# Performance work log

Hardware: AMD Instinct MI355X
Metric: run time of the kernel (lower is better)

## Reference

```python
import jax, jax.numpy as jnp
import numpy as np

B, S, D_MODEL, H = 2, 2048, 1024, 16
DIMS = D_MODEL // H  # 64


def setup_inputs() -> dict:
    key = jax.random.key(0)
    ks = jax.random.split(key, 7)
    scale = 1.0 / np.sqrt(D_MODEL)
    x = jax.random.normal(ks[0], (B, S, D_MODEL), dtype=jnp.float32)
    # Stacked per-head projection params: nn.Linear(d_model, dims) per head
    Wq = jax.random.uniform(ks[1], (H, DIMS, D_MODEL), minval=-scale, maxval=scale, dtype=jnp.float32)
    Wk = jax.random.uniform(ks[2], (H, DIMS, D_MODEL), minval=-scale, maxval=scale, dtype=jnp.float32)
    Wv = jax.random.uniform(ks[3], (H, DIMS, D_MODEL), minval=-scale, maxval=scale, dtype=jnp.float32)
    bq = jax.random.uniform(ks[4], (H, DIMS), minval=-scale, maxval=scale, dtype=jnp.float32)
    bk = jax.random.uniform(ks[5], (H, DIMS), minval=-scale, maxval=scale, dtype=jnp.float32)
    bv = jax.random.uniform(ks[6], (H, DIMS), minval=-scale, maxval=scale, dtype=jnp.float32)
    return {"x": x, "Wq": Wq, "Wk": Wk, "Wv": Wv, "bq": bq, "bk": bk, "bv": bv}


def reference(x, Wq, Wk, Wv, bq, bk, bv):
    # Per-head linear projections: [B,S,D] x [H,E,D] -> [B,H,S,E]
    q = jnp.einsum('bsd,hed->bhse', x, Wq) + bq[None, :, None, :]
    k = jnp.einsum('bsd,hed->bhse', x, Wk) + bk[None, :, None, :]
    v = jnp.einsum('bsd,hed->bhse', x, Wv) + bv[None, :, None, :]
    norm = DIMS ** (-0.5)
    # (q @ k^T) * norm @ v  -- NO softmax, as in the source
    scores = jnp.einsum('bhse,bhte->bhst', q, k) * norm  # [B,H,S,S]
    out = jnp.einsum('bhst,bhte->bhse', scores, v)       # [B,H,S,E]
    # concat heads along feature dim (head order matches torch.cat)
    return out.transpose(0, 2, 1, 3).reshape(B, S, H * DIMS)
```

## Files before the change

kernel.cpp:

```cpp
#include <hip/hip_runtime.h>


typedef __attribute__((ext_vector_type(8))) __bf16 bf16x8;
typedef __attribute__((ext_vector_type(8))) short short8;
typedef __attribute__((ext_vector_type(4))) float f32x4;
typedef __attribute__((ext_vector_type(4))) unsigned short ushort4v;

#define NX  4194304
#define NW1 1048576
#define NW  3145728

__device__ __forceinline__ float bf2f(unsigned short u) {
  union { unsigned int i; float f; } v; v.i = ((unsigned int)u) << 16; return v.f;
}
__device__ __forceinline__ unsigned short f2bf(float f) {
  union { float f; unsigned int i; } v; v.f = f;
  unsigned int u = v.i;
  u += 0x7fffu + ((u >> 16) & 1u);
  return (unsigned short)(u >> 16);
}

__device__ __forceinline__ void gload_lds16(const void* g, void* l) {
  __builtin_amdgcn_global_load_lds(
      (const __attribute__((address_space(1))) void*)(unsigned long long)(g),
      (__attribute__((address_space(3))) void*)(unsigned int)(unsigned long long)(l),
      16, 0, 0);
}

__global__ __launch_bounds__(256) void convert_pack(
    const float* __restrict__ x,
    const float* __restrict__ wq, const float* __restrict__ wk,
    const float* __restrict__ wv,
    const float* __restrict__ bq, const float* __restrict__ bk,
    const float* __restrict__ bv,
    unsigned short* __restrict__ Xbf, unsigned short* __restrict__ Wcat,
    float* __restrict__ Bcat)
{
  const long long t8 = ((long long)blockIdx.x * 256 + threadIdx.x) * 8;
  const float* src;
  unsigned short* dst;
  long long off;
  if (t8 < NX) {
    src = x; dst = Xbf; off = t8;
  } else if (t8 < NX + NW) {
    const long long w = t8 - NX;
    const int z = (int)(w >> 20);
    off = w & (NW1 - 1);
    src = (z == 0) ? wq : (z == 1) ? wk : wv;
    dst = Wcat + (long long)z * NW1;
  } else if (t8 < NX + NW + 3072) {
    const long long bo = t8 - (NX + NW);
    const int z = (int)(bo >> 10);
    const long long o2 = bo & 1023;
    const float* bsrc = (z == 0) ? bq : (z == 1) ? bk : bv;
    *(f32x4*)(Bcat + z * 1024 + o2)     = *(const f32x4*)(bsrc + o2);
    *(f32x4*)(Bcat + z * 1024 + o2 + 4) = *(const f32x4*)(bsrc + o2 + 4);
    return;
  } else {
    return;
  }
  f32x4 v0 = *(const f32x4*)(src + off);
  f32x4 v1 = *(const f32x4*)(src + off + 4);
  union { short8 s; unsigned short u[8]; } o;
#pragma unroll
  for (int j = 0; j < 4; ++j) {
    o.u[j]     = f2bf(v0[j]);
    o.u[4 + j] = f2bf(v1[j]);
  }
  *(short8*)(dst + off) = o.s;
}

#define ABYTES 32768
#define BBYTES 24576
#define BUFB   57344
__global__ __launch_bounds__(512, 2) void qkv_gemm(
    const unsigned short* __restrict__ Xbf,
    const unsigned short* __restrict__ Wcat,
    const float* __restrict__ Bcat,
    unsigned short* __restrict__ Qt,
    unsigned short* __restrict__ Kt,
    unsigned short* __restrict__ Vt)
{
  __shared__ unsigned char lds[2 * BUFB];

  const int tid = threadIdx.x;
  int bid = blockIdx.x;
  bid = (bid & 7) * 32 + (bid >> 3);
  const int colBase = (bid & 15) * 192;
  const int rowBase = (bid >> 4) * 256;

  const int lane = tid & 63;
  const int wid  = tid >> 6;
  const int wm = wid >> 2;
  const int wn = wid & 3;
  const int wr = wm * 128;
  const int wc = wn * 48;
  const int lr = lane & 15;
  const int lk = lane >> 4;

  const int sArow[4] = { (0*512+tid) >> 3, (1*512+tid) >> 3,
                         (2*512+tid) >> 3, (3*512+tid) >> 3 };
  const int sseg = tid & 7;

  f32x4 acc[8][3] = {};

#define STAGE(buf, kt)                                                        \
  {                                                                           \
    const int k0_ = (kt) * 64;                                                \
    _Pragma("unroll")                                                         \
    for (int i_ = 0; i_ < 4; ++i_) {                                          \
      const int row_ = sArow[i_];                                             \
      const int ss_ = sseg ^ (row_ & 7);                                      \
      gload_lds16(Xbf + (size_t)(rowBase + row_) * 1024 + k0_ + ss_ * 8,      \
                  lds + (buf) * BUFB + (i_ * 512 + tid) * 16);                \
    }                                                                         \
    _Pragma("unroll")                                                         \
    for (int i_ = 0; i_ < 3; ++i_) {                                          \
      const int row_ = sArow[i_];                                             \
      const int ss_ = sseg ^ (row_ & 7);                                      \
      gload_lds16(Wcat + (size_t)(colBase + row_) * 1024 + k0_ + ss_ * 8,     \
                  lds + (buf) * BUFB + ABYTES + (i_ * 512 + tid) * 16);       \
    }                                                                         \
  }

  STAGE(0, 0);
  STAGE(1, 1);
  asm volatile("s_waitcnt vmcnt(7)" ::: "memory");
  __builtin_amdgcn_s_barrier();

  for (int t = 0; t < 16; ++t) {
    const int cur = t & 1;
    const unsigned char* Ab = lds + cur * BUFB;
    const unsigned char* Bb = Ab + ABYTES;

    bf16x8 af[2][8], bvf[2][3];
#pragma unroll
    for (int ks = 0; ks < 2; ++ks) {
#pragma unroll
      for (int m = 0; m < 8; ++m) {
        const int row = wr + m * 16 + lr;
        af[ks][m] = *(const bf16x8*)(Ab + row * 128 +
                                     (((ks * 4 + lk) ^ (row & 7)) * 16));
      }
#pragma unroll
      for (int n = 0; n < 3; ++n) {
        const int row = wc + n * 16 + lr;
        bvf[ks][n] = *(const bf16x8*)(Bb + row * 128 +
                                      (((ks * 4 + lk) ^ (row & 7)) * 16));
      }
    }
    asm volatile("s_waitcnt lgkmcnt(0)" ::: "memory");
    __builtin_amdgcn_s_barrier();

    if (t + 2 < 16) STAGE(cur, t + 2);

#pragma unroll
    for (int ks = 0; ks < 2; ++ks)
#pragma unroll
      for (int m = 0; m < 8; ++m)
#pragma unroll
        for (int n = 0; n < 3; ++n)
          acc[m][n] = __builtin_amdgcn_mfma_f32_16x16x32_bf16(
              af[ks][m], bvf[ks][n], acc[m][n], 0, 0, 0);

    if (t < 13) asm volatile("s_waitcnt vmcnt(7)" ::: "memory");
    else        asm volatile("s_waitcnt vmcnt(0)" ::: "memory");
    __builtin_amdgcn_s_barrier();
  }
#undef STAGE

  const int bB = rowBase >> 11;
#pragma unroll
  for (int n = 0; n < 3; ++n) {
    const int colG = colBase + wc + n * 16 + lr;
    const float bval = Bcat[colG];
    const int zone = colG >> 10;
    unsigned short* __restrict__ T = (zone == 0) ? Qt : (zone == 1) ? Kt : Vt;
    const int hf = (colG >> 6) & 15;
    const int f  = colG & 63;
    const size_t rowOff = ((size_t)(bB * 16 + hf) * 64 + f) * 2048;
#pragma unroll
    for (int m = 0; m < 8; ++m) {
      const int t = (rowBase + wr + m * 16 + lk * 4) & 2047;
      ushort4v pk;
#pragma unroll
      for (int j = 0; j < 4; ++j)
        pk[j] = f2bf(acc[m][n][j] + bval);
      *(ushort4v*)&T[rowOff + t] = pk;
    }
  }
}

__global__ __launch_bounds__(64) void kv_outer(
    const unsigned short* __restrict__ Kt,
    const unsigned short* __restrict__ Vt,
    float* __restrict__ Mpart)
{
  const int lane = threadIdx.x;
  const int blk = blockIdx.x;
  const int bh = blk >> 3, tc = blk & 7;
  const int lr = lane & 15, lk = lane >> 4;
  const size_t base = (size_t)bh * 64 * 2048;

  f32x4 acc[4][4] = {};
#pragma unroll
  for (int ks = 0; ks < 8; ++ks) {
    const int t0 = tc * 256 + ks * 32 + lk * 8;
    bf16x8 af[4], bf[4];
#pragma unroll
    for (int m = 0; m < 4; ++m)
      af[m] = *(const bf16x8*)&Kt[base + (size_t)(m * 16 + lr) * 2048 + t0];
#pragma unroll
    for (int n = 0; n < 4; ++n)
      bf[n] = *(const bf16x8*)&Vt[base + (size_t)(n * 16 + lr) * 2048 + t0];
#pragma unroll
    for (int m = 0; m < 4; ++m)
#pragma unroll
      for (int n = 0; n < 4; ++n)
        acc[m][n] = __builtin_amdgcn_mfma_f32_16x16x32_bf16(af[m], bf[n], acc[m][n], 0, 0, 0);
  }
  float* out = Mpart + (size_t)blk * 4096;
#pragma unroll
  for (int m = 0; m < 4; ++m)
#pragma unroll
    for (int n = 0; n < 4; ++n)
#pragma unroll
      for (int j = 0; j < 4; ++j)
        out[(m * 16 + lk * 4 + j) * 64 + n * 16 + lr] = acc[m][n][j];
}

__global__ __launch_bounds__(256) void qm_out(
    const unsigned short* __restrict__ Qt, const float* __restrict__ Mpart,
    float* __restrict__ Out)
{
  __shared__ float Ms[64 * 64];
  __shared__ float Qst[64 * 132];
  const int tid = threadIdx.x;
  const int b = blockIdx.z, h = blockIdx.y, s0 = blockIdx.x * 128;
  const int bh = b * 16 + h;

#pragma unroll
  for (int i = 0; i < 4; ++i) {
    const int off = i * 1024 + tid * 4;
    f32x4 s = {};
#pragma unroll
    for (int ch = 0; ch < 8; ++ch)
      s += *(const f32x4*)&Mpart[((size_t)bh * 8 + ch) * 4096 + off];
    s *= 0.125f;
    *(f32x4*)&Ms[off] = s;
  }
  const size_t qbase = (size_t)bh * 64 * 2048;
#pragma unroll
  for (int i = 0; i < 4; ++i) {
    const int slot = i * 256 + tid;
    const int f = slot >> 4, c = slot & 15;
    short8 q = *(const short8*)&Qt[qbase + (size_t)f * 2048 + s0 + c * 8];
#pragma unroll
    for (int j = 0; j < 8; ++j)
      Qst[f * 132 + c * 8 + j] = bf2f((unsigned short)q[j]);
  }
  __syncthreads();

  const int s = (tid >> 3) * 4;
  const int e0 = (tid & 7) * 8;
  float acc2[4][8] = {};
  for (int f = 0; f < 64; ++f) {
    f32x4 m0 = *(const f32x4*)&Ms[f * 64 + e0];
    f32x4 m1 = *(const f32x4*)&Ms[f * 64 + e0 + 4];
#pragma unroll
    for (int i = 0; i < 4; ++i) {
      const float q = Qst[f * 132 + s + i];
#pragma unroll
      for (int j = 0; j < 4; ++j) {
        acc2[i][j]     += q * m0[j];
        acc2[i][j + 4] += q * m1[j];
      }
    }
  }
  const size_t obase = ((size_t)b * 2048 + s0) * 1024 + h * 64;
#pragma unroll
  for (int i = 0; i < 4; ++i) {
    f32x4 o0 = { acc2[i][0], acc2[i][1], acc2[i][2], acc2[i][3] };
    f32x4 o1 = { acc2[i][4], acc2[i][5], acc2[i][6], acc2[i][7] };
    *(f32x4*)&Out[obase + (size_t)(s + i) * 1024 + e0]     = o0;
    *(f32x4*)&Out[obase + (size_t)(s + i) * 1024 + e0 + 4] = o1;
  }
}

extern "C" void kernel_launch(void* const* d_in, const int* in_sizes, int n_in,
                              void* d_out, int out_size, void* d_ws, size_t ws_size,
                              hipStream_t stream) {
  const float* x  = (const float*)d_in[0];
  const float* Wq = (const float*)d_in[1];
  const float* Wk = (const float*)d_in[2];
  const float* Wv = (const float*)d_in[3];
  const float* bq = (const float*)d_in[4];
  const float* bk = (const float*)d_in[5];
  const float* bv = (const float*)d_in[6];
  float* out = (float*)d_out;

  char* ws = (char*)d_ws;
  const size_t MiB = 1024ull * 1024ull;
  unsigned short* Xbf   = (unsigned short*)(ws);
  unsigned short* Wcat  = (unsigned short*)(ws + 8  * MiB);
  float*          Bcat  = (float*)         (ws + 14 * MiB);
  unsigned short* Qt    = (unsigned short*)(ws + 15 * MiB);
  unsigned short* Kt    = (unsigned short*)(ws + 23 * MiB);
  unsigned short* Vt    = (unsigned short*)(ws + 31 * MiB);
  float*          Mpart = (float*)         (ws + 39 * MiB);

  convert_pack<<<3586, 256, 0, stream>>>(x, Wq, Wk, Wv, bq, bk, bv,
                                         Xbf, Wcat, Bcat);
  qkv_gemm<<<256, 512, 0, stream>>>(Xbf, Wcat, Bcat, Qt, Kt, Vt);
  kv_outer<<<256, 64, 0, stream>>>(Kt, Vt, Mpart);
  qm_out<<<dim3(16, 16, 2), 256, 0, stream>>>(Qt, Mpart, out);
}
```

Before: 66.95 us.

## Halve QKV GEMM row tile and use triple-buffered interleaved LDS pipeline

The QKV projection GEMM tile shrinks from 256 to 128 rows, doubling the grid to 512 blocks so more CUs are busy. The LDS pipeline becomes a three-buffer ring, and the global-to-LDS loads for the stage two steps ahead are split across the two k-substeps so they interleave with MFMA work. MFMA blocks are wrapped in s_setprio raises. The change trades more redundant loading of weight tiles and more barriers for better occupancy and latency hiding.

```diff
diff --git a/kernel.cpp b/kernel.cpp
--- a/kernel.cpp
+++ b/kernel.cpp
@@ -70,9 +70,7 @@
   *(short8*)(dst + off) = o.s;
 }
 
-#define ABYTES 32768
-#define BBYTES 24576
-#define BUFB   57344
+#define TBUF 40960
 __global__ __launch_bounds__(512, 2) void qkv_gemm(
     const unsigned short* __restrict__ Xbf,
     const unsigned short* __restrict__ Wcat,
@@ -81,93 +79,104 @@
     unsigned short* __restrict__ Kt,
     unsigned short* __restrict__ Vt)
 {
-  __shared__ unsigned char lds[2 * BUFB];
+  __shared__ unsigned char lds[3 * TBUF];
 
   const int tid = threadIdx.x;
   int bid = blockIdx.x;
-  bid = (bid & 7) * 32 + (bid >> 3);
+  bid = (bid & 7) * 64 + (bid >> 3);
   const int colBase = (bid & 15) * 192;
-  const int rowBase = (bid >> 4) * 256;
+  const int rowBase = (bid >> 4) * 128;
 
   const int lane = tid & 63;
   const int wid  = tid >> 6;
   const int wm = wid >> 2;
   const int wn = wid & 3;
-  const int wr = wm * 128;
+  const int wr = wm * 64;
   const int wc = wn * 48;
   const int lr = lane & 15;
   const int lk = lane >> 4;
 
-  const int sArow[4] = { (0*512+tid) >> 3, (1*512+tid) >> 3,
-                         (2*512+tid) >> 3, (3*512+tid) >> 3 };
+  const int sr0 = tid >> 3;
+  const int sr1 = (512 + tid) >> 3;
+  const int sr2 = (1024 + tid) >> 3;
   const int sseg = tid & 7;
-
-  f32x4 acc[8][3] = {};
-
-#define STAGE(buf, kt)                                                        \
-  {                                                                           \
-    const int k0_ = (kt) * 64;                                                \
-    _Pragma("unroll")                                                         \
-    for (int i_ = 0; i_ < 4; ++i_) {                                          \
-      const int row_ = sArow[i_];                                             \
-      const int ss_ = sseg ^ (row_ & 7);                                      \
-      gload_lds16(Xbf + (size_t)(rowBase + row_) * 1024 + k0_ + ss_ * 8,      \
-                  lds + (buf) * BUFB + (i_ * 512 + tid) * 16);                \
-    }                                                                         \
-    _Pragma("unroll")                                                         \
-    for (int i_ = 0; i_ < 3; ++i_) {                                          \
-      const int row_ = sArow[i_];                                             \
-      const int ss_ = sseg ^ (row_ & 7);                                      \
-      gload_lds16(Wcat + (size_t)(colBase + row_) * 1024 + k0_ + ss_ * 8,     \
-                  lds + (buf) * BUFB + ABYTES + (i_ * 512 + tid) * 16);       \
-    }                                                                         \
-  }
-
-  STAGE(0, 0);
-  STAGE(1, 1);
-  asm volatile("s_waitcnt vmcnt(7)" ::: "memory");
+  const int dbase = (tid & ~63) * 16;
+
+  f32x4 acc[4][3] = {};
+
+#pragma unroll
+  for (int p = 0; p < 2; ++p) {
+    unsigned char* Sb = lds + p * TBUF;
+    const int k2 = p * 64;
+    gload_lds16(Xbf + (size_t)(rowBase + sr0) * 1024 + k2 + (sseg ^ (sr0 & 7)) * 8,
+                Sb + dbase);
+    gload_lds16(Xbf + (size_t)(rowBase + sr1) * 1024 + k2 + (sseg ^ (sr1 & 7)) * 8,
+                Sb + 8192 + dbase);
+    gload_lds16(Wcat + (size_t)(colBase + sr0) * 1024 + k2 + (sseg ^ (sr0 & 7)) * 8,
+                Sb + 16384 + dbase);
+    gload_lds16(Wcat + (size_t)(colBase + sr1) * 1024 + k2 + (sseg ^ (sr1 & 7)) * 8,
+                Sb + 24576 + dbase);
+    gload_lds16(Wcat + (size_t)(colBase + sr2) * 1024 + k2 + (sseg ^ (sr2 & 7)) * 8,
+                Sb + 32768 + dbase);
+  }
+  asm volatile("s_waitcnt vmcnt(5)" ::: "memory");
   __builtin_amdgcn_s_barrier();
 
-  for (int t = 0; t < 16; ++t) {
-    const int cur = t & 1;
-    const unsigned char* Ab = lds + cur * BUFB;
-    const unsigned char* Bb = Ab + ABYTES;
-
-    bf16x8 af[2][8], bvf[2][3];
+  for (int j = 0; j < 16; ++j) {
+    const unsigned char* Ab = lds + (j % 3) * TBUF;
+    const unsigned char* Bb = Ab + 16384;
+    const int js = j + 2;
+    const bool doStage = (js < 16);
+    unsigned char* Sb = lds + (js % 3) * TBUF;
+    const int k2 = js * 64;
+
 #pragma unroll
     for (int ks = 0; ks < 2; ++ks) {
-#pragma unroll
-      for (int m = 0; m < 8; ++m) {
+      bf16x8 af[4], bv[3];
+#pragma unroll
+      for (int m = 0; m < 4; ++m) {
         const int row = wr + m * 16 + lr;
-        af[ks][m] = *(const bf16x8*)(Ab + row * 128 +
-                                     (((ks * 4 + lk) ^ (row & 7)) * 16));
+        af[m] = *(const bf16x8*)(Ab + row * 128 +
+                                 (((ks * 4 + lk) ^ (row & 7)) * 16));
       }
 #pragma unroll
       for (int n = 0; n < 3; ++n) {
         const int row = wc + n * 16 + lr;
-        bvf[ks][n] = *(const bf16x8*)(Bb + row * 128 +
-                                      (((ks * 4 + lk) ^ (row & 7)) * 16));
-      }
-    }
-    asm volatile("s_waitcnt lgkmcnt(0)" ::: "memory");
-    __builtin_amdgcn_s_barrier();
-
-    if (t + 2 < 16) STAGE(cur, t + 2);
-
-#pragma unroll
-    for (int ks = 0; ks < 2; ++ks)
-#pragma unroll
-      for (int m = 0; m < 8; ++m)
+        bv[n] = *(const bf16x8*)(Bb + row * 128 +
+                                 (((ks * 4 + lk) ^ (row & 7)) * 16));
+      }
+      if (doStage) {
+        if (ks == 0) {
+          gload_lds16(Xbf + (size_t)(rowBase + sr0) * 1024 + k2 + (sseg ^ (sr0 & 7)) * 8,
+                      Sb + dbase);
+          gload_lds16(Xbf + (size_t)(rowBase + sr1) * 1024 + k2 + (sseg ^ (sr1 & 7)) * 8,
+                      Sb + 8192 + dbase);
+          gload_lds16(Wcat + (size_t)(colBase + sr0) * 1024 + k2 + (sseg ^ (sr0 & 7)) * 8,
+                      Sb + 16384 + dbase);
+        } else {
+          gload_lds16(Wcat + (size_t)(colBase + sr1) * 1024 + k2 + (sseg ^ (sr1 & 7)) * 8,
+                      Sb + 24576 + dbase);
+          gload_lds16(Wcat + (size_t)(colBase + sr2) * 1024 + k2 + (sseg ^ (sr2 & 7)) * 8,
+                      Sb + 32768 + dbase);
+        }
+      }
+      __builtin_amdgcn_s_barrier();
+      asm volatile("s_waitcnt lgkmcnt(0)" ::: "memory");
+      __builtin_amdgcn_s_setprio(1);
+#pragma unroll
+      for (int m = 0; m < 4; ++m)
 #pragma unroll
         for (int n = 0; n < 3; ++n)
           acc[m][n] = __builtin_amdgcn_mfma_f32_16x16x32_bf16(
-              af[ks][m], bvf[ks][n], acc[m][n], 0, 0, 0);
-
-    if (t < 13) asm volatile("s_waitcnt vmcnt(7)" ::: "memory");
-    else        asm volatile("s_waitcnt vmcnt(0)" ::: "memory");
-    __builtin_amdgcn_s_barrier();
-  }
-#undef STAGE
+              af[m], bv[n], acc[m][n], 0, 0, 0);
+      __builtin_amdgcn_s_setprio(0);
+      if (ks == 1) {
+        if (j < 14)       asm volatile("s_waitcnt vmcnt(5)" ::: "memory");
+        else if (j == 14) asm volatile("s_waitcnt vmcnt(0)" ::: "memory");
+      }
+      __builtin_amdgcn_s_barrier();
+    }
+  }
 
   const int bB = rowBase >> 11;
 #pragma unroll
@@ -180,12 +189,12 @@
     const int f  = colG & 63;
     const size_t rowOff = ((size_t)(bB * 16 + hf) * 64 + f) * 2048;
 #pragma unroll
-    for (int m = 0; m < 8; ++m) {
+    for (int m = 0; m < 4; ++m) {
       const int t = (rowBase + wr + m * 16 + lk * 4) & 2047;
       ushort4v pk;
 #pragma unroll
-      for (int j = 0; j < 4; ++j)
-        pk[j] = f2bf(acc[m][n][j] + bval);
+      for (int jj = 0; jj < 4; ++jj)
+        pk[jj] = f2bf(acc[m][n][jj] + bval);
       *(ushort4v*)&T[rowOff + t] = pk;
     }
   }
@@ -311,7 +320,7 @@
 
   convert_pack<<<3586, 256, 0, stream>>>(x, Wq, Wk, Wv, bq, bk, bv,
                                          Xbf, Wcat, Bcat);
-  qkv_gemm<<<256, 512, 0, stream>>>(Xbf, Wcat, Bcat, Qt, Kt, Vt);
+  qkv_gemm<<<512, 512, 0, stream>>>(Xbf, Wcat, Bcat, Qt, Kt, Vt);
   kv_outer<<<256, 64, 0, stream>>>(Kt, Vt, Mpart);
   qm_out<<<dim3(16, 16, 2), 256, 0, stream>>>(Qt, Mpart, out);
 }
```

Result: slower. 70.95 us (+6.0%).

## Restructure QKV GEMM mainloop into 4-stage K32 pipeline with split loaders

Applied to the files above, without the earlier changes.

The QKV projection GEMM now walks K in 32-wide steps through a four-buffer LDS ring with three stages in flight instead of 64-wide steps with double buffering. Half the threads load the X tile and half load the W tile, with precomputed global pointers and a new XOR swizzle. Each step needs only one barrier instead of two, and the MFMA block runs at raised wave priority. The aim is to hide global-load latency and cut barrier overhead, at the cost of more loop iterations, per-thread vmcnt bookkeeping that differs between the two loader groups, and more care needed to keep the waits correct.

```diff
diff --git a/kernel.cpp b/kernel.cpp
--- a/kernel.cpp
+++ b/kernel.cpp
@@ -70,9 +70,9 @@
   *(short8*)(dst + off) = o.s;
 }
 
-#define ABYTES 32768
-#define BBYTES 24576
-#define BUFB   57344
+#define ABUF_B 16384
+#define BBUF_B 12288
+#define TILE_B 28672
 __global__ __launch_bounds__(512, 2) void qkv_gemm(
     const unsigned short* __restrict__ Xbf,
     const unsigned short* __restrict__ Wcat,
@@ -81,7 +81,7 @@
     unsigned short* __restrict__ Kt,
     unsigned short* __restrict__ Vt)
 {
-  __shared__ unsigned char lds[2 * BUFB];
+  __shared__ unsigned char lds[4 * TILE_B];
 
   const int tid = threadIdx.x;
   int bid = blockIdx.x;
@@ -91,82 +91,68 @@
 
   const int lane = tid & 63;
   const int wid  = tid >> 6;
-  const int wm = wid >> 2;
-  const int wn = wid & 3;
-  const int wr = wm * 128;
-  const int wc = wn * 48;
+  const int wr = (wid >> 2) * 128;
+  const int wc = (wid & 3) * 48;
   const int lr = lane & 15;
   const int lk = lane >> 4;
-
-  const int sArow[4] = { (0*512+tid) >> 3, (1*512+tid) >> 3,
-                         (2*512+tid) >> 3, (3*512+tid) >> 3 };
-  const int sseg = tid & 7;
+  const int fofs = (lk ^ ((lr >> 1) & 3)) << 4;
+
+  const bool isA = (tid < 256);
+  const int tloc = isA ? tid : (tid - 256);
+
+  const unsigned short* gptr[4];
+  int lofs[4];
+#pragma unroll
+  for (int l = 0; l < 4; ++l) {
+    const int unit = l * 256 + tloc;
+    const int row  = unit >> 2;
+    const int sc   = ((unit & 3) ^ ((row >> 1) & 3)) << 3;
+    const int rowc = (!isA && row > 191) ? 0 : row;
+    gptr[l] = isA ? (Xbf  + (size_t)(rowBase + rowc) * 1024 + sc)
+                  : (Wcat + (size_t)(colBase + rowc) * 1024 + sc);
+    lofs[l] = (isA ? 0 : ABUF_B) + unit * 16;
+  }
 
   f32x4 acc[8][3] = {};
 
-#define STAGE(buf, kt)                                                        \
-  {                                                                           \
-    const int k0_ = (kt) * 64;                                                \
-    _Pragma("unroll")                                                         \
-    for (int i_ = 0; i_ < 4; ++i_) {                                          \
-      const int row_ = sArow[i_];                                             \
-      const int ss_ = sseg ^ (row_ & 7);                                      \
-      gload_lds16(Xbf + (size_t)(rowBase + row_) * 1024 + k0_ + ss_ * 8,      \
-                  lds + (buf) * BUFB + (i_ * 512 + tid) * 16);                \
-    }                                                                         \
-    _Pragma("unroll")                                                         \
-    for (int i_ = 0; i_ < 3; ++i_) {                                          \
-      const int row_ = sArow[i_];                                             \
-      const int ss_ = sseg ^ (row_ & 7);                                      \
-      gload_lds16(Wcat + (size_t)(colBase + row_) * 1024 + k0_ + ss_ * 8,     \
-                  lds + (buf) * BUFB + ABYTES + (i_ * 512 + tid) * 16);       \
-    }                                                                         \
-  }
-
-  STAGE(0, 0);
-  STAGE(1, 1);
-  asm volatile("s_waitcnt vmcnt(7)" ::: "memory");
-  __builtin_amdgcn_s_barrier();
-
-  for (int t = 0; t < 16; ++t) {
-    const int cur = t & 1;
-    const unsigned char* Ab = lds + cur * BUFB;
-    const unsigned char* Bb = Ab + ABYTES;
-
-    bf16x8 af[2][8], bvf[2][3];
-#pragma unroll
-    for (int ks = 0; ks < 2; ++ks) {
-#pragma unroll
-      for (int m = 0; m < 8; ++m) {
-        const int row = wr + m * 16 + lr;
-        af[ks][m] = *(const bf16x8*)(Ab + row * 128 +
-                                     (((ks * 4 + lk) ^ (row & 7)) * 16));
-      }
-#pragma unroll
-      for (int n = 0; n < 3; ++n) {
-        const int row = wc + n * 16 + lr;
-        bvf[ks][n] = *(const bf16x8*)(Bb + row * 128 +
-                                      (((ks * 4 + lk) ^ (row & 7)) * 16));
-      }
-    }
-    asm volatile("s_waitcnt lgkmcnt(0)" ::: "memory");
-    __builtin_amdgcn_s_barrier();
-
-    if (t + 2 < 16) STAGE(cur, t + 2);
-
-#pragma unroll
-    for (int ks = 0; ks < 2; ++ks)
-#pragma unroll
-      for (int m = 0; m < 8; ++m)
-#pragma unroll
-        for (int n = 0; n < 3; ++n)
-          acc[m][n] = __builtin_amdgcn_mfma_f32_16x16x32_bf16(
-              af[ks][m], bvf[ks][n], acc[m][n], 0, 0, 0);
-
-    if (t < 13) asm volatile("s_waitcnt vmcnt(7)" ::: "memory");
-    else        asm volatile("s_waitcnt vmcnt(0)" ::: "memory");
-    __builtin_amdgcn_s_barrier();
-  }
+#define STAGE(j3)                                                    \
+  { unsigned char* Sb_ = lds + ((j3) & 3) * TILE_B;                  \
+    const int ko_ = (j3) * 32;                                       \
+    if (isA) {                                                       \
+      _Pragma("unroll") for (int l = 0; l < 4; ++l)                  \
+        gload_lds16(gptr[l] + ko_, Sb_ + lofs[l]);                   \
+    } else {                                                         \
+      _Pragma("unroll") for (int l = 0; l < 3; ++l)                  \
+        gload_lds16(gptr[l] + ko_, Sb_ + lofs[l]);                   \
+    } }
+
+#define KSTEP(j, DOSTAGE, VMA, VMB)                                       \
+  { if (isA) asm volatile("s_waitcnt vmcnt(" #VMA ")" ::: "memory");      \
+    else     asm volatile("s_waitcnt vmcnt(" #VMB ")" ::: "memory");      \
+    asm volatile("s_barrier" ::: "memory");                               \
+    const unsigned char* Ab_ = lds + ((j) & 3) * TILE_B;                  \
+    const unsigned char* Bb_ = Ab_ + ABUF_B;                              \
+    bf16x8 a_[8], b_[3];                                                  \
+    _Pragma("unroll") for (int m = 0; m < 8; ++m)                         \
+      a_[m] = *(const bf16x8*)(Ab_ + (wr + m * 16 + lr) * 64 + fofs);     \
+    _Pragma("unroll") for (int n = 0; n < 3; ++n)                         \
+      b_[n] = *(const bf16x8*)(Bb_ + (wc + n * 16 + lr) * 64 + fofs);     \
+    if (DOSTAGE) STAGE((j) + 3);                                          \
+    __builtin_amdgcn_s_setprio(1);                                        \
+    _Pragma("unroll") for (int m = 0; m < 8; ++m)                         \
+      _Pragma("unroll") for (int n = 0; n < 3; ++n)                       \
+        acc[m][n] = __builtin_amdgcn_mfma_f32_16x16x32_bf16(              \
+            a_[m], b_[n], acc[m][n], 0, 0, 0);                            \
+    __builtin_amdgcn_s_setprio(0);                                        \
+  }
+
+  STAGE(0); STAGE(1); STAGE(2);
+
+  for (int j = 0; j < 29; ++j) KSTEP(j, true, 8, 6);
+  KSTEP(29, false, 8, 6);
+  KSTEP(30, false, 4, 3);
+  KSTEP(31, false, 0, 0);
+#undef KSTEP
 #undef STAGE
 
   const int bB = rowBase >> 11;
@@ -184,8 +170,8 @@
       const int t = (rowBase + wr + m * 16 + lk * 4) & 2047;
       ushort4v pk;
 #pragma unroll
-      for (int j = 0; j < 4; ++j)
-        pk[j] = f2bf(acc[m][n][j] + bval);
+      for (int jj = 0; jj < 4; ++jj)
+        pk[jj] = f2bf(acc[m][n][jj] + bval);
       *(ushort4v*)&T[rowOff + t] = pk;
     }
   }
```

New measurement: 66.50 us. Within noise of the previous version (-0.7%).
